# Performance work log

Hardware: AMD Instinct MI355X
Metric: run time of the kernel (lower is better)

The kernel has to match this reference:

```python
import jax, jax.numpy as jnp
import numpy as np

N_NODES = 50000
N_EDGES = 800000
D_IN, H1, H2, N_CLASSES = 128, 128, 64, 2


def setup_inputs() -> dict:
    key = jax.random.key(0)
    ks = jax.random.split(key, 8)
    x = jax.random.normal(ks[0], (N_NODES, D_IN), dtype=jnp.float32)
    edge_index = jax.random.randint(ks[1], (2, N_EDGES), 0, N_NODES, dtype=jnp.int64)
    s = 1.0 / np.sqrt(D_IN)
    W1 = jax.random.uniform(ks[2], (D_IN, H1), jnp.float32, -s, s)
    b1 = jnp.zeros((H1,), jnp.float32)
    s = 1.0 / np.sqrt(H1)
    W2 = jax.random.uniform(ks[3], (H1, H2), jnp.float32, -s, s)
    b2 = jnp.zeros((H2,), jnp.float32)
    s = 1.0 / np.sqrt(H2)
    Wo = jax.random.uniform(ks[4], (H2, N_CLASSES), jnp.float32, -s, s)
    bo = jax.random.uniform(ks[5], (N_CLASSES,), jnp.float32, -s, s)
    return {"x": x, "edge_index": edge_index, "W1": W1, "b1": b1,
            "W2": W2, "b2": b2, "Wo": Wo, "bo": bo}


def _gcn_conv(x, W, b, src, dst, n_nodes):
    # PyG GCNConv: add self loops, symmetric normalization deg^{-1/2} A deg^{-1/2}
    h = x @ W  # [N, out]
    ones = jnp.ones((src.shape[0],), h.dtype)
    deg = jax.ops.segment_sum(ones, dst, num_segments=n_nodes) + 1.0  # +1 self loop
    dinv = jax.lax.rsqrt(deg)  # deg >= 1 always (self loops)
    coef = dinv[src] * dinv[dst]  # [E]
    msg = h[src] * coef[:, None]  # [E, out] gather
    agg = jax.ops.segment_sum(msg, dst, num_segments=n_nodes)  # scatter-add
    agg = agg + h * (dinv * dinv)[:, None]  # self-loop contribution
    return agg + b


def reference(x, edge_index, W1, b1, W2, b2, Wo, bo):
    src, dst = edge_index[0], edge_index[1]
    n = x.shape[0]
    h = jax.nn.relu(_gcn_conv(x, W1, b1, src, dst, n))
    # dropout p=0.25 is identity in eval mode
    h = jax.nn.relu(_gcn_conv(h, W2, b2, src, dst, n))
    logits = h @ Wo + bo
    return jax.nn.log_softmax(logits, axis=1)
```

## Files before the change

### kernel.cpp

```cpp
#include <hip/hip_runtime.h>
#include <stdint.h>

#define N_NODES 50000
#define N_EDGES 800000
#define CAP 80
#define ZROW N_NODES

typedef __attribute__((ext_vector_type(8))) short short8;
typedef __attribute__((ext_vector_type(4))) float floatx4;

__device__ __forceinline__ float bflo(uint32_t u) { return __uint_as_float(u << 16); }
__device__ __forceinline__ float bfhi(uint32_t u) { return __uint_as_float(u & 0xffff0000u); }
__device__ __forceinline__ unsigned short f2b(float f) {
    uint32_t u = __float_as_uint(f);
    u += 0x7fffu + ((u >> 16) & 1u);
    return (unsigned short)(u >> 16);
}

__global__ void k_prep(const float* __restrict__ W1, const float* __restrict__ W2,
                       unsigned short* __restrict__ Wt1, unsigned short* __restrict__ Wt2,
                       int* __restrict__ counts) {
    int gid = blockIdx.x * 256 + threadIdx.x;
    if (gid < 16384) {
        int k = gid >> 7, n = gid & 127;
        Wt1[n * 128 + k] = f2b(W1[gid]);
    } else if (gid < 24576) {
        int j = gid - 16384;
        int k = j >> 6, n = j & 63;
        Wt2[n * 128 + k] = f2b(W2[j]);
    } else if (gid < 24576 + N_NODES) {
        counts[gid - 24576] = 0;
    }
}

__global__ __launch_bounds__(256) void k_scat(const int* __restrict__ src,
                                              const int* __restrict__ dst,
                                              int* __restrict__ counts,
                                              int* __restrict__ csr) {
    int i = blockIdx.x * 256 + threadIdx.x;
    if (i >= N_EDGES / 8) return;
    const int4* s4 = (const int4*)(src + i * 8);
    const int4* d4 = (const int4*)(dst + i * 8);
    int4 sa = s4[0], sb = s4[1];
    int4 da = d4[0], db = d4[1];
    int r0 = atomicAdd(&counts[da.x], 1);
    int r1 = atomicAdd(&counts[da.y], 1);
    int r2 = atomicAdd(&counts[da.z], 1);
    int r3 = atomicAdd(&counts[da.w], 1);
    int r4 = atomicAdd(&counts[db.x], 1);
    int r5 = atomicAdd(&counts[db.y], 1);
    int r6 = atomicAdd(&counts[db.z], 1);
    int r7 = atomicAdd(&counts[db.w], 1);
    if (r0 < CAP) csr[da.x * CAP + r0] = sa.x;
    if (r1 < CAP) csr[da.y * CAP + r1] = sa.y;
    if (r2 < CAP) csr[da.z * CAP + r2] = sa.z;
    if (r3 < CAP) csr[da.w * CAP + r3] = sa.w;
    if (r4 < CAP) csr[db.x * CAP + r4] = sb.x;
    if (r5 < CAP) csr[db.y * CAP + r5] = sb.y;
    if (r6 < CAP) csr[db.z * CAP + r6] = sb.z;
    if (r7 < CAP) csr[db.w * CAP + r7] = sb.w;
}

__global__ __launch_bounds__(256) void k_gemm1(const float* __restrict__ x,
                                               const unsigned short* __restrict__ Wt1,
                                               const int* __restrict__ counts,
                                               unsigned short* __restrict__ h1s,
                                               unsigned short* __restrict__ h2s) {
    __shared__ unsigned short At[64 * 136];
    __shared__ unsigned short Bt[128 * 136];
    int t = threadIdx.x;
    int row0 = blockIdx.x * 64;
    for (int i = t; i < 2048; i += 256) {
        int n = i >> 4, kc = (i & 15) * 8;
        *(uint4*)&Bt[n * 136 + kc] = *(const uint4*)(Wt1 + n * 128 + kc);
    }
    for (int i = t; i < 1024; i += 256) {
        int r = i >> 4, kc = (i & 15) * 8;
        int g = row0 + r; if (g >= N_NODES) g = N_NODES - 1;
        const float* p = x + g * 128 + kc;
        float4 a = *(const float4*)p, b = *(const float4*)(p + 4);
        uint4 o;
        o.x = (uint32_t)f2b(a.x) | ((uint32_t)f2b(a.y) << 16);
        o.y = (uint32_t)f2b(a.z) | ((uint32_t)f2b(a.w) << 16);
        o.z = (uint32_t)f2b(b.x) | ((uint32_t)f2b(b.y) << 16);
        o.w = (uint32_t)f2b(b.z) | ((uint32_t)f2b(b.w) << 16);
        *(uint4*)&At[r * 136 + kc] = o;
    }
    __syncthreads();
    int wv = t >> 6, lane = t & 63;
    int m = lane & 15, qd = lane >> 4;
    floatx4 acc[8];
    #pragma unroll
    for (int c = 0; c < 8; c++) acc[c] = (floatx4){0.f, 0.f, 0.f, 0.f};
    const unsigned short* ap = &At[(wv * 16 + m) * 136 + qd * 8];
    const unsigned short* bp = &Bt[m * 136 + qd * 8];
    #pragma unroll
    for (int kk = 0; kk < 4; kk++) {
        short8 af = *(const short8*)(ap + kk * 32);
        #pragma unroll
        for (int c = 0; c < 8; c++) {
            short8 bf = *(const short8*)(bp + c * 16 * 136 + kk * 32);
            acc[c] = __builtin_amdgcn_mfma_f32_16x16x32_bf16(af, bf, acc[c], 0, 0, 0);
        }
    }
    #pragma unroll
    for (int reg = 0; reg < 4; reg++) {
        int g = row0 + wv * 16 + qd * 4 + reg;
        if (g < N_NODES) {
            float di = rsqrtf((float)counts[g] + 1.0f);
            #pragma unroll
            for (int c = 0; c < 8; c++)
                h1s[g * 128 + c * 16 + m] = f2b(di * acc[c][reg]);
        } else {
            #pragma unroll
            for (int c = 0; c < 8; c++)
                h1s[g * 128 + c * 16 + m] = 0;
            #pragma unroll
            for (int c = 0; c < 4; c++)
                h2s[g * 64 + c * 16 + m] = 0;
        }
    }
}

__global__ __launch_bounds__(256) void k_agg1g2(const unsigned short* __restrict__ h1s,
                                                const unsigned short* __restrict__ Wt2,
                                                const int* __restrict__ csr,
                                                const int* __restrict__ counts,
                                                const float* __restrict__ b1,
                                                unsigned short* __restrict__ h2s) {
    __shared__ unsigned short Bt[64 * 136];
    __shared__ unsigned short At[16 * 136];
    int t = threadIdx.x;
    for (int i = t; i < 1024; i += 256) {
        int n = i >> 4, kc = (i & 15) * 8;
        *(uint4*)&Bt[n * 136 + kc] = *(const uint4*)(Wt2 + n * 128 + kc);
    }
    int wv = t >> 6, lane = t & 63;
    int q = lane >> 4, l = lane & 15;
    int v0 = blockIdx.x * 16;
    int v = v0 + wv * 4 + q;
    int n = counts[v];
    float dv = rsqrtf((float)n + 1.0f);
    int n_eff = min(n, CAP);
    const int* cs = csr + v * CAP;
    int nmax = n_eff;
    nmax = max(nmax, __shfl_xor(nmax, 16));
    nmax = max(nmax, __shfl_xor(nmax, 32));
    float a0, a1, a2, a3, a4, a5, a6, a7;
    {
        uint4 p = *(const uint4*)(h1s + v * 128 + l * 8);
        a0 = bflo(p.x); a1 = bfhi(p.x); a2 = bflo(p.y); a3 = bfhi(p.y);
        a4 = bflo(p.z); a5 = bfhi(p.z); a6 = bflo(p.w); a7 = bfhi(p.w);
    }
    for (int base = 0; base < nmax; base += 16) {
        int idx = base + l;
        int e = (idx < n_eff) ? cs[idx] : ZROW;
        int mm = nmax - base; if (mm > 16) mm = 16;
        #pragma unroll 4
        for (int i = 0; i < mm; i++) {
            int s = __shfl(e, (q << 4) + i);
            uint4 p = *(const uint4*)(h1s + s * 128 + l * 8);
            a0 += bflo(p.x); a1 += bfhi(p.x); a2 += bflo(p.y); a3 += bfhi(p.y);
            a4 += bflo(p.z); a5 += bfhi(p.z); a6 += bflo(p.w); a7 += bfhi(p.w);
        }
    }
    {
        float4 bL = *(const float4*)(b1 + l * 8);
        float4 bH = *(const float4*)(b1 + l * 8 + 4);
        a0 = fmaxf(fmaf(dv, a0, bL.x), 0.f); a1 = fmaxf(fmaf(dv, a1, bL.y), 0.f);
        a2 = fmaxf(fmaf(dv, a2, bL.z), 0.f); a3 = fmaxf(fmaf(dv, a3, bL.w), 0.f);
        a4 = fmaxf(fmaf(dv, a4, bH.x), 0.f); a5 = fmaxf(fmaf(dv, a5, bH.y), 0.f);
        a6 = fmaxf(fmaf(dv, a6, bH.z), 0.f); a7 = fmaxf(fmaf(dv, a7, bH.w), 0.f);
        uint4 o;
        o.x = (uint32_t)f2b(a0) | ((uint32_t)f2b(a1) << 16);
        o.y = (uint32_t)f2b(a2) | ((uint32_t)f2b(a3) << 16);
        o.z = (uint32_t)f2b(a4) | ((uint32_t)f2b(a5) << 16);
        o.w = (uint32_t)f2b(a6) | ((uint32_t)f2b(a7) << 16);
        *(uint4*)&At[(wv * 4 + q) * 136 + l * 8] = o;
    }
    __syncthreads();
    int m = lane & 15, qd = lane >> 4;
    floatx4 acc = (floatx4){0.f, 0.f, 0.f, 0.f};
    const unsigned short* ap = &At[m * 136 + qd * 8];
    const unsigned short* bp = &Bt[(wv * 16 + m) * 136 + qd * 8];
    #pragma unroll
    for (int kk = 0; kk < 4; kk++) {
        short8 af = *(const short8*)(ap + kk * 32);
        short8 bf = *(const short8*)(bp + kk * 32);
        acc = __builtin_amdgcn_mfma_f32_16x16x32_bf16(af, bf, acc, 0, 0, 0);
    }
    #pragma unroll
    for (int reg = 0; reg < 4; reg++) {
        int g = v0 + qd * 4 + reg;
        float dg = rsqrtf((float)counts[g] + 1.0f);
        h2s[g * 64 + wv * 16 + m] = f2b(dg * acc[reg]);
    }
}

__global__ __launch_bounds__(256) void k_agg2(const unsigned short* __restrict__ h2s,
                                              const int* __restrict__ csr,
                                              const int* __restrict__ counts,
                                              const float* __restrict__ b2,
                                              const float* __restrict__ Wo,
                                              const float* __restrict__ bo,
                                              float* __restrict__ out) {
    int wave = (blockIdx.x * 256 + threadIdx.x) >> 6;
    int lane = threadIdx.x & 63;
    int q = lane >> 4, l = lane & 15;
    int v = wave * 4 + q;
    int n = counts[v];
    float dv = rsqrtf((float)n + 1.0f);
    int n_eff = min(n, CAP);
    const int* cs = csr + v * CAP;
    int nmax = n_eff;
    nmax = max(nmax, __shfl_xor(nmax, 16));
    nmax = max(nmax, __shfl_xor(nmax, 32));
    float a0, a1, a2, a3;
    {
        uint2 p = *(const uint2*)(h2s + v * 64 + l * 4);
        a0 = bflo(p.x); a1 = bfhi(p.x); a2 = bflo(p.y); a3 = bfhi(p.y);
    }
    for (int base = 0; base < nmax; base += 16) {
        int idx = base + l;
        int e = (idx < n_eff) ? cs[idx] : ZROW;
        int mm = nmax - base; if (mm > 16) mm = 16;
        #pragma unroll 4
        for (int i = 0; i < mm; i++) {
            int s = __shfl(e, (q << 4) + i);
            uint2 p = *(const uint2*)(h2s + s * 64 + l * 4);
            a0 += bflo(p.x); a1 += bfhi(p.x); a2 += bflo(p.y); a3 += bfhi(p.y);
        }
    }
    float4 bb = *(const float4*)(b2 + l * 4);
    a0 = fmaxf(fmaf(dv, a0, bb.x), 0.f);
    a1 = fmaxf(fmaf(dv, a1, bb.y), 0.f);
    a2 = fmaxf(fmaf(dv, a2, bb.z), 0.f);
    a3 = fmaxf(fmaf(dv, a3, bb.w), 0.f);
    float4 w01 = *(const float4*)(Wo + l * 8);
    float4 w23 = *(const float4*)(Wo + l * 8 + 4);
    float l0 = a0 * w01.x + a1 * w01.z + a2 * w23.x + a3 * w23.z;
    float l1 = a0 * w01.y + a1 * w01.w + a2 * w23.y + a3 * w23.w;
    #pragma unroll
    for (int off = 8; off > 0; off >>= 1) {
        l0 += __shfl_xor(l0, off);
        l1 += __shfl_xor(l1, off);
    }
    if (l == 0) {
        float2 bof = *(const float2*)bo;
        l0 += bof.x; l1 += bof.y;
        float m = fmaxf(l0, l1);
        float ls = m + __logf(__expf(l0 - m) + __expf(l1 - m));
        *(float2*)(out + v * 2) = make_float2(l0 - ls, l1 - ls);
    }
}

extern "C" void kernel_launch(void* const* d_in, const int* in_sizes, int n_in,
                              void* d_out, int out_size, void* d_ws, size_t ws_size,
                              hipStream_t stream) {
    const float* x  = (const float*)d_in[0];
    const int* ei   = (const int*)d_in[1];
    const float* W1 = (const float*)d_in[2];
    const float* b1 = (const float*)d_in[3];
    const float* W2 = (const float*)d_in[4];
    const float* b2 = (const float*)d_in[5];
    const float* Wo = (const float*)d_in[6];
    const float* bo = (const float*)d_in[7];
    float* out      = (float*)d_out;
    const int* src = ei;
    const int* dst = ei + N_EDGES;

    char* w = (char*)d_ws;
    int* counts = (int*)(w + 0);
    int* csr    = (int*)(w + 200704);
    unsigned short* Wt1 = (unsigned short*)(w + 16200704);
    unsigned short* Wt2 = (unsigned short*)(w + 16233472);
    unsigned short* h1s = (unsigned short*)(w + 16249856);
    unsigned short* h2s = (unsigned short*)(w + 29062144);

    k_prep  <<<292, 256, 0, stream>>>(W1, W2, Wt1, Wt2, counts);
    k_scat  <<<391, 256, 0, stream>>>(src, dst, counts, csr);
    k_gemm1 <<<782, 256, 0, stream>>>(x, Wt1, counts, h1s, h2s);
    k_agg1g2<<<3125, 256, 0, stream>>>(h1s, Wt2, csr, counts, b1, h2s);
    k_agg2  <<<3125, 256, 0, stream>>>(h2s, csr, counts, b2, Wo, bo, out);
}
```

Baseline: 195.6 us.

## Fuse edge scatter with first GEMM by deferring source degree scaling to aggregation

Merges the CSR-building scatter kernel and the first-layer GEMM into one launch, where blocks are split by index into scatter and GEMM roles. To drop the GEMM's dependence on the degree counts, the source-side deg^-1/2 factor is no longer applied in the GEMM. It is instead computed per neighbor in the aggregation kernel, from a counts gather and a shuffle, and applied with FMAs. This saves a launch and lets the atomic scatter overlap with the matrix multiply, at the cost of an extra counts read and rsqrt per neighbor in the aggregation. The prep kernel also drops its bounds check so it now zeroes the padding entries of counts, including the sentinel row used by the aggregation.

```diff
diff --git a/kernel.cpp b/kernel.cpp
--- a/kernel.cpp
+++ b/kernel.cpp
@@ -5,6 +5,8 @@
 #define N_EDGES 800000
 #define CAP 80
 #define ZROW N_NODES
+#define SCAT_BLOCKS 391
+#define GEMM_BLOCKS 782
 
 typedef __attribute__((ext_vector_type(8))) short short8;
 typedef __attribute__((ext_vector_type(4))) float floatx4;
@@ -28,48 +30,48 @@
         int j = gid - 16384;
         int k = j >> 6, n = j & 63;
         Wt2[n * 128 + k] = f2b(W2[j]);
-    } else if (gid < 24576 + N_NODES) {
+    } else {
         counts[gid - 24576] = 0;
     }
 }
 
-__global__ __launch_bounds__(256) void k_scat(const int* __restrict__ src,
-                                              const int* __restrict__ dst,
-                                              int* __restrict__ counts,
-                                              int* __restrict__ csr) {
-    int i = blockIdx.x * 256 + threadIdx.x;
-    if (i >= N_EDGES / 8) return;
-    const int4* s4 = (const int4*)(src + i * 8);
-    const int4* d4 = (const int4*)(dst + i * 8);
-    int4 sa = s4[0], sb = s4[1];
-    int4 da = d4[0], db = d4[1];
-    int r0 = atomicAdd(&counts[da.x], 1);
-    int r1 = atomicAdd(&counts[da.y], 1);
-    int r2 = atomicAdd(&counts[da.z], 1);
-    int r3 = atomicAdd(&counts[da.w], 1);
-    int r4 = atomicAdd(&counts[db.x], 1);
-    int r5 = atomicAdd(&counts[db.y], 1);
-    int r6 = atomicAdd(&counts[db.z], 1);
-    int r7 = atomicAdd(&counts[db.w], 1);
-    if (r0 < CAP) csr[da.x * CAP + r0] = sa.x;
-    if (r1 < CAP) csr[da.y * CAP + r1] = sa.y;
-    if (r2 < CAP) csr[da.z * CAP + r2] = sa.z;
-    if (r3 < CAP) csr[da.w * CAP + r3] = sa.w;
-    if (r4 < CAP) csr[db.x * CAP + r4] = sb.x;
-    if (r5 < CAP) csr[db.y * CAP + r5] = sb.y;
-    if (r6 < CAP) csr[db.z * CAP + r6] = sb.z;
-    if (r7 < CAP) csr[db.w * CAP + r7] = sb.w;
-}
-
-__global__ __launch_bounds__(256) void k_gemm1(const float* __restrict__ x,
-                                               const unsigned short* __restrict__ Wt1,
-                                               const int* __restrict__ counts,
-                                               unsigned short* __restrict__ h1s,
-                                               unsigned short* __restrict__ h2s) {
+__global__ __launch_bounds__(256) void k_scat_gemm1(const int* __restrict__ src,
+                                                    const int* __restrict__ dst,
+                                                    int* __restrict__ counts,
+                                                    int* __restrict__ csr,
+                                                    const float* __restrict__ x,
+                                                    const unsigned short* __restrict__ Wt1,
+                                                    unsigned short* __restrict__ h1s,
+                                                    unsigned short* __restrict__ h2s) {
     __shared__ unsigned short At[64 * 136];
     __shared__ unsigned short Bt[128 * 136];
     int t = threadIdx.x;
-    int row0 = blockIdx.x * 64;
+    if (blockIdx.x < SCAT_BLOCKS) {
+        int i = blockIdx.x * 256 + t;
+        if (i >= N_EDGES / 8) return;
+        const int4* s4 = (const int4*)(src + i * 8);
+        const int4* d4 = (const int4*)(dst + i * 8);
+        int4 sa = s4[0], sb = s4[1];
+        int4 da = d4[0], db = d4[1];
+        int r0 = atomicAdd(&counts[da.x], 1);
+        int r1 = atomicAdd(&counts[da.y], 1);
+        int r2 = atomicAdd(&counts[da.z], 1);
+        int r3 = atomicAdd(&counts[da.w], 1);
+        int r4 = atomicAdd(&counts[db.x], 1);
+        int r5 = atomicAdd(&counts[db.y], 1);
+        int r6 = atomicAdd(&counts[db.z], 1);
+        int r7 = atomicAdd(&counts[db.w], 1);
+        if (r0 < CAP) csr[da.x * CAP + r0] = sa.x;
+        if (r1 < CAP) csr[da.y * CAP + r1] = sa.y;
+        if (r2 < CAP) csr[da.z * CAP + r2] = sa.z;
+        if (r3 < CAP) csr[da.w * CAP + r3] = sa.w;
+        if (r4 < CAP) csr[db.x * CAP + r4] = sb.x;
+        if (r5 < CAP) csr[db.y * CAP + r5] = sb.y;
+        if (r6 < CAP) csr[db.z * CAP + r6] = sb.z;
+        if (r7 < CAP) csr[db.w * CAP + r7] = sb.w;
+        return;
+    }
+    int row0 = (blockIdx.x - SCAT_BLOCKS) * 64;
     for (int i = t; i < 2048; i += 256) {
         int n = i >> 4, kc = (i & 15) * 8;
         *(uint4*)&Bt[n * 136 + kc] = *(const uint4*)(Wt1 + n * 128 + kc);
@@ -107,10 +109,9 @@
     for (int reg = 0; reg < 4; reg++) {
         int g = row0 + wv * 16 + qd * 4 + reg;
         if (g < N_NODES) {
-            float di = rsqrtf((float)counts[g] + 1.0f);
             #pragma unroll
             for (int c = 0; c < 8; c++)
-                h1s[g * 128 + c * 16 + m] = f2b(di * acc[c][reg]);
+                h1s[g * 128 + c * 16 + m] = f2b(acc[c][reg]);
         } else {
             #pragma unroll
             for (int c = 0; c < 8; c++)
@@ -149,19 +150,23 @@
     float a0, a1, a2, a3, a4, a5, a6, a7;
     {
         uint4 p = *(const uint4*)(h1s + v * 128 + l * 8);
-        a0 = bflo(p.x); a1 = bfhi(p.x); a2 = bflo(p.y); a3 = bfhi(p.y);
-        a4 = bflo(p.z); a5 = bfhi(p.z); a6 = bflo(p.w); a7 = bfhi(p.w);
+        a0 = dv * bflo(p.x); a1 = dv * bfhi(p.x); a2 = dv * bflo(p.y); a3 = dv * bfhi(p.y);
+        a4 = dv * bflo(p.z); a5 = dv * bfhi(p.z); a6 = dv * bflo(p.w); a7 = dv * bfhi(p.w);
     }
     for (int base = 0; base < nmax; base += 16) {
         int idx = base + l;
         int e = (idx < n_eff) ? cs[idx] : ZROW;
+        float de = rsqrtf((float)counts[e] + 1.0f);
         int mm = nmax - base; if (mm > 16) mm = 16;
         #pragma unroll 4
         for (int i = 0; i < mm; i++) {
             int s = __shfl(e, (q << 4) + i);
+            float di = __shfl(de, (q << 4) + i);
             uint4 p = *(const uint4*)(h1s + s * 128 + l * 8);
-            a0 += bflo(p.x); a1 += bfhi(p.x); a2 += bflo(p.y); a3 += bfhi(p.y);
-            a4 += bflo(p.z); a5 += bfhi(p.z); a6 += bflo(p.w); a7 += bfhi(p.w);
+            a0 = fmaf(di, bflo(p.x), a0); a1 = fmaf(di, bfhi(p.x), a1);
+            a2 = fmaf(di, bflo(p.y), a2); a3 = fmaf(di, bfhi(p.y), a3);
+            a4 = fmaf(di, bflo(p.z), a4); a5 = fmaf(di, bfhi(p.z), a5);
+            a6 = fmaf(di, bflo(p.w), a6); a7 = fmaf(di, bfhi(p.w), a7);
         }
     }
     {
@@ -277,9 +282,9 @@
     unsigned short* h1s = (unsigned short*)(w + 16249856);
     unsigned short* h2s = (unsigned short*)(w + 29062144);
 
-    k_prep  <<<292, 256, 0, stream>>>(W1, W2, Wt1, Wt2, counts);
-    k_scat  <<<391, 256, 0, stream>>>(src, dst, counts, csr);
-    k_gemm1 <<<782, 256, 0, stream>>>(x, Wt1, counts, h1s, h2s);
-    k_agg1g2<<<3125, 256, 0, stream>>>(h1s, Wt2, csr, counts, b1, h2s);
-    k_agg2  <<<3125, 256, 0, stream>>>(h2s, csr, counts, b2, Wo, bo, out);
-}
+    k_prep      <<<292, 256, 0, stream>>>(W1, W2, Wt1, Wt2, counts);
+    k_scat_gemm1<<<SCAT_BLOCKS + GEMM_BLOCKS, 256, 0, stream>>>(src, dst, counts, csr,
+                                                                x, Wt1, h1s, h2s);
+    k_agg1g2    <<<3125, 256, 0, stream>>>(h1s, Wt2, csr, counts, b1, h2s);
+    k_agg2      <<<3125, 256, 0, stream>>>(h2s, csr, counts, b2, Wo, bo, out);
+}
```

Measured after the change: 186.8 us. 4.5% less time.
